# Performance work log

Hardware: AMD Instinct MI355X
Metric: run time of the kernel (lower is better)

## Reference

```python
import jax, jax.numpy as jnp
import numpy as np

EMBED_DIM = 768
NUM_HEADS = 12
HEAD_DIM = EMBED_DIM // NUM_HEADS
SCALE = HEAD_DIM ** -0.5
B, N = 8, 1024


def setup_inputs() -> dict:
    key = jax.random.key(0)
    ks = jax.random.split(key, 5)
    return {
        "x": jax.random.normal(ks[0], (B, N, EMBED_DIM), dtype=jnp.float32),
        "qkv_w": jax.random.normal(ks[1], (3 * EMBED_DIM, EMBED_DIM), dtype=jnp.float32) * 0.02,
        "qkv_b": jax.random.normal(ks[2], (3 * EMBED_DIM,), dtype=jnp.float32) * 0.02,
        "proj_w": jax.random.normal(ks[3], (EMBED_DIM, EMBED_DIM), dtype=jnp.float32) * 0.02,
        "proj_b": jax.random.normal(ks[4], (EMBED_DIM,), dtype=jnp.float32) * 0.02,
    }


def reference(x, qkv_w, qkv_b, proj_w, proj_b):
    b, n, c = x.shape
    h, hd = NUM_HEADS, HEAD_DIM
    # QKV projection: [b,n,3c]
    qkv = jnp.einsum("bnc,dc->bnd", x, qkv_w) + qkv_b
    qkv = qkv.reshape(b, n, 3, h, hd).transpose(2, 0, 3, 1, 4)  # [3,b,h,n,hd]
    q, k, v = qkv[0], qkv[1], qkv[2]
    # scaled dot-product attention (eager path; dropout is identity in eval)
    attn = jnp.einsum("bhqd,bhkd->bhqk", q, k) * SCALE
    attn = jax.nn.softmax(attn, axis=-1)
    out = jnp.einsum("bhqk,bhkd->bhqd", attn, v)  # [b,h,n,hd]
    out = out.transpose(0, 2, 1, 3).reshape(b, n, c)
    # output projection
    return jnp.einsum("bnc,dc->bnd", out, proj_w) + proj_b
```

## Files before the change

### kernel.cpp

```cpp
#include <hip/hip_runtime.h>
#include <hip/hip_bf16.h>

typedef __attribute__((ext_vector_type(4))) float f32x4;
typedef __attribute__((ext_vector_type(8))) short short8;
typedef unsigned short u16;

#define MFMA(a, b, c) __builtin_amdgcn_mfma_f32_16x16x32_bf16((a), (b), (c), 0, 0, 0)

#define WAITVM_BAR(N) do {                                          \
    asm volatile("s_waitcnt vmcnt(" #N ")" ::: "memory");           \
    __builtin_amdgcn_s_barrier();                                   \
    __builtin_amdgcn_sched_barrier(0);                              \
} while (0)
#define BAR2() do {                                                 \
    __builtin_amdgcn_sched_barrier(0);                              \
    __builtin_amdgcn_s_barrier();                                   \
    __builtin_amdgcn_sched_barrier(0);                              \
} while (0)

static constexpr int EMBED = 768;
static constexpr int NH = 12;
static constexpr int HD = 64;
static constexpr int BATCH = 8;
static constexpr int SEQ = 1024;

__device__ __forceinline__ u16 f2bu(float f) {
    __hip_bfloat16 h = __float2bfloat16(f);
    u16 u; __builtin_memcpy(&u, &h, 2); return u;
}
__device__ __forceinline__ float exp2a(float x) {
    float r; asm("v_exp_f32 %0, %1" : "=v"(r) : "v"(x)); return r;
}
__device__ __forceinline__ unsigned cvt_pk_bf16(float lo, float hi) {
    unsigned r; asm("v_cvt_pk_bf16_f32 %0, %1, %2" : "=v"(r) : "v"(lo), "v"(hi)); return r;
}
__device__ __forceinline__ float max3f(float a, float b, float c) {
    return fmaxf(fmaxf(a, b), c);
}
__device__ __forceinline__ void swap32(unsigned& a, unsigned& b) {
    asm volatile("v_permlane32_swap_b32 %0, %1" : "+v"(a), "+v"(b));
}
__device__ __forceinline__ void swap16(unsigned& a, unsigned& b) {
    asm volatile("v_permlane16_swap_b32 %0, %1" : "+v"(a), "+v"(b));
}
__device__ __forceinline__ short8 mk8(unsigned w0, unsigned w1, unsigned w2, unsigned w3) {
    union { unsigned u[4]; short8 s; } c;
    c.u[0] = w0; c.u[1] = w1; c.u[2] = w2; c.u[3] = w3;
    return c.s;
}

__global__ void cvt_all_k(const float* __restrict__ x, const float* __restrict__ w1,
                          const float* __restrict__ w2,
                          u16* __restrict__ xb, u16* __restrict__ wb, u16* __restrict__ pw) {
    const int n1 = BATCH * SEQ * EMBED;
    const int n2 = 3 * EMBED * EMBED;
    const int n3 = EMBED * EMBED;
    int i = (blockIdx.x * blockDim.x + threadIdx.x) * 4;
    const float* src; u16* dst;
    if (i < n1)            { src = x  + i;             dst = xb + i; }
    else if (i < n1 + n2)  { src = w1 + (i - n1);      dst = wb + (i - n1); }
    else if (i < n1+n2+n3) { src = w2 + (i - n1 - n2); dst = pw + (i - n1 - n2); }
    else return;
    float4 v = *reinterpret_cast<const float4*>(src);
    ushort4 o;
    o.x = f2bu(v.x); o.y = f2bu(v.y); o.z = f2bu(v.z); o.w = f2bu(v.w);
    *reinterpret_cast<ushort4*>(dst) = o;
}

template <int EPI>
__global__ __launch_bounds__(256)
void gemm_bt_k(const u16* __restrict__ A, const u16* __restrict__ Bw,
               const float* __restrict__ bias,
               u16* __restrict__ q_out, u16* __restrict__ k_out,
               u16* __restrict__ vt_out, float* __restrict__ f_out)
{
    __shared__ __attribute__((aligned(16))) char smem[65536];
    const int tid  = threadIdx.x;
    const int wave = tid >> 6, lane = tid & 63;
    const int hi   = lane >> 4, l15 = lane & 15;
    const int wr   = wave >> 1, wc = wave & 1;
    const int bm   = blockIdx.x, bn = blockIdx.y;

    f32x4 acc[4][4] = {};

    const size_t arow0 = (size_t)bm * 128;
    const size_t brow0 = (size_t)bn * 128;

    auto stage = [&](int buf, int kt) {
        char* Ab = smem + buf * 32768;
        char* Bb = Ab + 16384;
#pragma unroll
        for (int c = 0; c < 4; ++c) {
            int ck   = c * 4 + wave;
            int p    = ck * 1024 + lane * 16;
            int row  = p >> 7;
            int pcol = (p & 127) ^ ((row & 7) << 4);
            const u16* srcA = A  + (arow0 + row) * EMBED + kt + (pcol >> 1);
            const u16* srcB = Bw + (brow0 + row) * EMBED + kt + (pcol >> 1);
            __builtin_amdgcn_global_load_lds((const __attribute__((address_space(1))) void*)srcA,
                                             (__attribute__((address_space(3))) void*)(Ab + ck * 1024), 16, 0, 0);
            __builtin_amdgcn_global_load_lds((const __attribute__((address_space(1))) void*)srcB,
                                             (__attribute__((address_space(3))) void*)(Bb + ck * 1024), 16, 0, 0);
        }
    };

    auto comp = [&](const char* Ab, const char* Bb) {
#pragma unroll
        for (int kk = 0; kk < 2; ++kk) {
            short8 af[4], bf[4];
#pragma unroll
            for (int mi = 0; mi < 4; ++mi) {
                int R  = wr * 64 + mi * 16 + l15;
                int Cb = kk * 64 + hi * 16;
                af[mi] = *reinterpret_cast<const short8*>(Ab + R * 128 + (Cb ^ ((R & 7) << 4)));
            }
#pragma unroll
            for (int ni = 0; ni < 4; ++ni) {
                int R  = wc * 64 + ni * 16 + l15;
                int Cb = kk * 64 + hi * 16;
                bf[ni] = *reinterpret_cast<const short8*>(Bb + R * 128 + (Cb ^ ((R & 7) << 4)));
            }
#pragma unroll
            for (int mi = 0; mi < 4; ++mi)
#pragma unroll
                for (int ni = 0; ni < 4; ++ni)
                    acc[mi][ni] = MFMA(af[mi], bf[ni], acc[mi][ni]);
        }
    };

    const char* A0 = smem;
    const char* B0 = smem + 16384;
    const char* A1 = smem + 32768;
    const char* B1 = smem + 49152;

    stage(0, 0);
#pragma unroll
    for (int tt = 0; tt < 5; ++tt) {
        stage(1, (2 * tt + 1) * 64);
        WAITVM_BAR(8);
        comp(A0, B0);
        BAR2();
        stage(0, (2 * tt + 2) * 64);
        WAITVM_BAR(8);
        comp(A1, B1);
        BAR2();
    }
    stage(1, 11 * 64);
    WAITVM_BAR(8);
    comp(A0, B0);
    BAR2();
    WAITVM_BAR(0);
    comp(A1, B1);

#pragma unroll
    for (int mi = 0; mi < 4; ++mi) {
        int crow0 = bm * 128 + wr * 64 + mi * 16 + hi * 4;
#pragma unroll
        for (int ni = 0; ni < 4; ++ni) {
            int ccol = bn * 128 + wc * 64 + ni * 16 + l15;
            float bv = bias[ccol];
            if constexpr (EPI == 0) {
                int which = ccol / 768;
                int rem   = ccol - which * 768;
                int hh = rem >> 6, hd = rem & 63;
                int bb = crow0 >> 10, nn0 = crow0 & 1023;
                size_t bh = (size_t)(bb * NH + hh);
                if (which == 2) {
                    uint2 pk;
                    pk.x = cvt_pk_bf16(acc[mi][ni][0] + bv, acc[mi][ni][1] + bv);
                    pk.y = cvt_pk_bf16(acc[mi][ni][2] + bv, acc[mi][ni][3] + bv);
                    *reinterpret_cast<uint2*>(&vt_out[(bh * HD + hd) * SEQ + nn0]) = pk;
                } else if (which == 0) {
#pragma unroll
                    for (int r = 0; r < 4; ++r)
                        q_out[(bh * SEQ + nn0 + r) * HD + hd] =
                            f2bu((acc[mi][ni][r] + bv) * 0.18033688f);
                } else {
#pragma unroll
                    for (int r = 0; r < 4; ++r)
                        k_out[(bh * SEQ + nn0 + r) * HD + hd] = f2bu(acc[mi][ni][r] + bv);
                }
            } else {
#pragma unroll
                for (int r = 0; r < 4; ++r)
                    f_out[(size_t)(crow0 + r) * EMBED + ccol] = acc[mi][ni][r] + bv;
            }
        }
    }
}

__global__ __launch_bounds__(256, 3)
void attn_k(const u16* __restrict__ Q, const u16* __restrict__ K,
            const u16* __restrict__ Vt, u16* __restrict__ AO)
{
    __shared__ __attribute__((aligned(16))) u16 kv[3][8192];

    const int tid = threadIdx.x;
    const int w   = tid >> 6, lane = tid & 63;
    const int hi  = lane >> 4, l15 = lane & 15;
    const int f   = blockIdx.x;
    const int xcd = f & 7, i = f >> 3;
    const int bh  = xcd * 12 + (i % 12);
    const int q0w = (i / 12) * 128 + w * 32;

    const u16* Qh = Q  + (size_t)bh * SEQ * HD;
    const u16* Kh = K  + (size_t)bh * SEQ * HD;
    const u16* Vh = Vt + (size_t)bh * HD * SEQ;

    short8 qf[2][2];
#pragma unroll
    for (int qh = 0; qh < 2; ++qh)
#pragma unroll
        for (int dh = 0; dh < 2; ++dh)
            qf[qh][dh] = *reinterpret_cast<const short8*>(
                Qh + (size_t)(q0w + qh * 16 + l15) * HD + dh * 32 + hi * 8);
    __builtin_amdgcn_sched_barrier(0);

    const u16* sptr[4]; int doff[4]; int sadv[4];
#pragma unroll
    for (int c = 0; c < 4; ++c) {
        int ch = c * 4 + w;
        int mc = ch & 7;
        int p  = mc * 1024 + lane * 16;
        int row = p >> 7;
        int colb = (p & 127) ^ ((row & 7) << 4);
        if (ch < 8) { sptr[c] = Kh + (size_t)row * HD + (colb >> 1); sadv[c] = 64 * HD; doff[c] = mc * 512; }
        else        { sptr[c] = Vh + (size_t)row * SEQ + (colb >> 1); sadv[c] = 64;     doff[c] = 4096 + mc * 512; }
    }
    auto stage = [&](int buf, int t) {
#pragma unroll
        for (int c = 0; c < 4; ++c)
            __builtin_amdgcn_global_load_lds(
                (const __attribute__((address_space(1))) void*)(sptr[c] + (size_t)t * sadv[c]),
                (__attribute__((address_space(3))) void*)(&kv[buf][doff[c]]), 16, 0, 0);
    };

    stage(0, 0);
    stage(1, 1);

    f32x4 accO0[4] = {}, accO1[4] = {};
    float m0 = 0.f, m1 = 0.f, lp0 = 0.f, lp1 = 0.f;

    auto tile = [&](const u16* Kb, const u16* Vb, bool first) {
        f32x4 st0[4] = {}, st1[4] = {};
        __builtin_amdgcn_s_setprio(1);
#pragma unroll
        for (int kb = 0; kb < 4; ++kb) {
            int R  = kb * 16 + l15;
            int sw = (R & 7) << 4;
            short8 kf0 = *reinterpret_cast<const short8*>(Kb + R * 64 + (((hi * 16) ^ sw) >> 1));
            short8 kf1 = *reinterpret_cast<const short8*>(Kb + R * 64 + (((64 + hi * 16) ^ sw) >> 1));
            st0[kb] = MFMA(kf0, qf[0][0], st0[kb]);
            st0[kb] = MFMA(kf1, qf[0][1], st0[kb]);
            st1[kb] = MFMA(kf0, qf[1][0], st1[kb]);
            st1[kb] = MFMA(kf1, qf[1][1], st1[kb]);
        }
        __builtin_amdgcn_s_setprio(0);

        float a0 = max3f(st0[0][0], st0[0][1], st0[0][2]);
        float a1 = max3f(st0[0][3], st0[1][0], st0[1][1]);
        float a2 = max3f(st0[1][2], st0[1][3], st0[2][0]);
        float a3 = max3f(st0[2][1], st0[2][2], st0[2][3]);
        float a4 = max3f(st0[3][0], st0[3][1], st0[3][2]);
        float tm0 = fmaxf(max3f(a0, a1, a2), max3f(a3, a4, st0[3][3]));
        float b0 = max3f(st1[0][0], st1[0][1], st1[0][2]);
        float b1 = max3f(st1[0][3], st1[1][0], st1[1][1]);
        float b2 = max3f(st1[1][2], st1[1][3], st1[2][0]);
        float b3 = max3f(st1[2][1], st1[2][2], st1[2][3]);
        float b4 = max3f(st1[3][0], st1[3][1], st1[3][2]);
        float tm1 = fmaxf(max3f(b0, b1, b2), max3f(b3, b4, st1[3][3]));
        tm0 = fmaxf(tm0, __shfl_xor(tm0, 16, 64));
        tm0 = fmaxf(tm0, __shfl_xor(tm0, 32, 64));
        tm1 = fmaxf(tm1, __shfl_xor(tm1, 16, 64));
        tm1 = fmaxf(tm1, __shfl_xor(tm1, 32, 64));
        if (first) { m0 = tm0; m1 = tm1; }

        unsigned X0[4][2], X1[4][2];
#pragma unroll
        for (int kb = 0; kb < 4; ++kb) {
            float e0 = exp2a(st0[kb][0] - m0);
            float e1 = exp2a(st0[kb][1] - m0);
            float e2 = exp2a(st0[kb][2] - m0);
            float e3 = exp2a(st0[kb][3] - m0);
            lp0 += (e0 + e1) + (e2 + e3);
            X0[kb][0] = cvt_pk_bf16(e0, e1);
            X0[kb][1] = cvt_pk_bf16(e2, e3);
            float g0 = exp2a(st1[kb][0] - m1);
            float g1 = exp2a(st1[kb][1] - m1);
            float g2 = exp2a(st1[kb][2] - m1);
            float g3 = exp2a(st1[kb][3] - m1);
            lp1 += (g0 + g1) + (g2 + g3);
            X1[kb][0] = cvt_pk_bf16(g0, g1);
            X1[kb][1] = cvt_pk_bf16(g2, g3);
        }

        unsigned c0 = X0[0][0], d0 = X0[1][0];
        swap32(c0, d0); swap16(c0, d0);
        unsigned c1 = X0[0][1], d1 = X0[1][1];
        swap32(c1, d1); swap16(c1, d1);
        unsigned c2 = X0[2][0], d2 = X0[3][0];
        swap32(c2, d2); swap16(c2, d2);
        unsigned c3 = X0[2][1], d3 = X0[3][1];
        swap32(c3, d3); swap16(c3, d3);
        short8 pa00 = mk8(c0, c1, d0, d1);
        short8 pa01 = mk8(c2, c3, d2, d3);
        unsigned e0 = X1[0][0], f0 = X1[1][0];
        swap32(e0, f0); swap16(e0, f0);
        unsigned e1 = X1[0][1], f1 = X1[1][1];
        swap32(e1, f1); swap16(e1, f1);
        unsigned e2 = X1[2][0], f2 = X1[3][0];
        swap32(e2, f2); swap16(e2, f2);
        unsigned e3 = X1[2][1], f3 = X1[3][1];
        swap32(e3, f3); swap16(e3, f3);
        short8 pa10 = mk8(e0, e1, f0, f1);
        short8 pa11 = mk8(e2, e3, f2, f3);

        __builtin_amdgcn_s_setprio(1);
#pragma unroll
        for (int db = 0; db < 4; ++db) {
            int R  = db * 16 + l15;
            int sw = (R & 7) << 4;
            short8 vf0 = *reinterpret_cast<const short8*>(Vb + R * 64 + (((hi * 16) ^ sw) >> 1));
            short8 vf1 = *reinterpret_cast<const short8*>(Vb + R * 64 + (((64 + hi * 16) ^ sw) >> 1));
            accO0[db] = MFMA(vf0, pa00, accO0[db]);
            accO0[db] = MFMA(vf1, pa01, accO0[db]);
            accO1[db] = MFMA(vf0, pa10, accO1[db]);
            accO1[db] = MFMA(vf1, pa11, accO1[db]);
        }
        __builtin_amdgcn_s_setprio(0);

        if (!first && !__all((tm0 <= m0 + 8.f) && (tm1 <= m1 + 8.f))) {
            float mn0 = fmaxf(m0, tm0), mn1 = fmaxf(m1, tm1);
            float s0 = exp2a(m0 - mn0), s1 = exp2a(m1 - mn1);
            m0 = mn0; m1 = mn1;
            lp0 *= s0; lp1 *= s1;
#pragma unroll
            for (int db = 0; db < 4; ++db)
#pragma unroll
                for (int r = 0; r < 4; ++r) { accO0[db][r] *= s0; accO1[db][r] *= s1; }
        }
    };

    auto one = [&](int bc, int bs, int tn, bool ds, bool first) {
        asm volatile("s_waitcnt vmcnt(4)" ::: "memory");
        __builtin_amdgcn_s_barrier();
        __builtin_amdgcn_sched_barrier(0);
        if (ds) stage(bs, tn);
        tile(&kv[bc][0], &kv[bc][4096], first);
        __builtin_amdgcn_sched_barrier(0);
    };

    one(0, 2, 2, true, true);
    one(1, 0, 3, true, false);
    one(2, 1, 4, true, false);
    for (int g = 1; g < 5; ++g) {
        one(0, 2, 3 * g + 2, true, false);
        one(1, 0, 3 * g + 3, 3 * g + 3 <= 15, false);
        one(2, 1, 3 * g + 4, 3 * g + 4 <= 15, false);
    }
    asm volatile("s_waitcnt vmcnt(0)" ::: "memory");
    __builtin_amdgcn_s_barrier();
    __builtin_amdgcn_sched_barrier(0);
    tile(&kv[0][0], &kv[0][4096], false);

    lp0 += __shfl_xor(lp0, 16, 64);
    lp0 += __shfl_xor(lp0, 32, 64);
    lp1 += __shfl_xor(lp1, 16, 64);
    lp1 += __shfl_xor(lp1, 32, 64);
    float linv0 = 1.f / lp0, linv1 = 1.f / lp1;
    const int bb = bh / NH, hh = bh - bb * NH;
    size_t rowb0 = ((size_t)bb * SEQ + q0w + l15) * EMBED + hh * HD;
    size_t rowb1 = rowb0 + (size_t)16 * EMBED;
#pragma unroll
    for (int db = 0; db < 4; ++db) {
        uint2 pk0, pk1;
        pk0.x = cvt_pk_bf16(accO0[db][0] * linv0, accO0[db][1] * linv0);
        pk0.y = cvt_pk_bf16(accO0[db][2] * linv0, accO0[db][3] * linv0);
        pk1.x = cvt_pk_bf16(accO1[db][0] * linv1, accO1[db][1] * linv1);
        pk1.y = cvt_pk_bf16(accO1[db][2] * linv1, accO1[db][3] * linv1);
        *reinterpret_cast<uint2*>(&AO[rowb0 + db * 16 + hi * 4]) = pk0;
        *reinterpret_cast<uint2*>(&AO[rowb1 + db * 16 + hi * 4]) = pk1;
    }
}

extern "C" void kernel_launch(void* const* d_in, const int* in_sizes, int n_in,
                              void* d_out, int out_size, void* d_ws, size_t ws_size,
                              hipStream_t stream)
{
    const float* x      = (const float*)d_in[0];
    const float* qkv_w  = (const float*)d_in[1];
    const float* qkv_b  = (const float*)d_in[2];
    const float* proj_w = (const float*)d_in[3];
    const float* proj_b = (const float*)d_in[4];
    float* out = (float*)d_out;

    char* ws = (char*)d_ws;
    u16* xb  = (u16*)(ws);
    u16* wb  = (u16*)(ws + 12582912);
    u16* pw  = (u16*)(ws + 16121856);
    u16* qb  = (u16*)(ws + 17301504);
    u16* kb  = (u16*)(ws + 29884416);
    u16* vt  = (u16*)(ws + 42467328);
    u16* ao  = (u16*)(ws + 55050240);

    cvt_all_k<<<8448, 256, 0, stream>>>(x, qkv_w, proj_w, xb, wb, pw);

    gemm_bt_k<0><<<dim3(64, 18), 256, 0, stream>>>(xb, wb, qkv_b, qb, kb, vt, nullptr);
    attn_k<<<768, 256, 0, stream>>>(qb, kb, vt, ao);
    gemm_bt_k<1><<<dim3(64, 6), 256, 0, stream>>>(ao, pw, proj_b, nullptr, nullptr, nullptr, out);
}
```

Baseline: 103.3 us.

## Switch attention kernel to 32x32x16 bf16 MFMA tiles

The attention kernel now computes QK^T and PV with 32x32x16 MFMA instructions, so each wave handles 32 query rows in one fragment instead of two 16-row fragments. The softmax row-max and row-sum reductions shrink to a single cross-half shuffle, and the P repacking needs only permlane32 swaps. The goal is fewer MFMA issues, fewer K/V LDS fragment reads per FLOP and less softmax bookkeeping. In exchange each lane holds larger accumulator vectors, which raises register pressure, and the fragment and output index mapping must be right for the new layout.

```diff
diff --git a/kernel.cpp b/kernel.cpp
--- a/kernel.cpp
+++ b/kernel.cpp
@@ -2,10 +2,12 @@
 #include <hip/hip_bf16.h>
 
 typedef __attribute__((ext_vector_type(4))) float f32x4;
+typedef __attribute__((ext_vector_type(16))) float f32x16;
 typedef __attribute__((ext_vector_type(8))) short short8;
 typedef unsigned short u16;
 
 #define MFMA(a, b, c) __builtin_amdgcn_mfma_f32_16x16x32_bf16((a), (b), (c), 0, 0, 0)
+#define MFMA32(a, b, c) __builtin_amdgcn_mfma_f32_32x32x16_bf16((a), (b), (c), 0, 0, 0)
 
 #define WAITVM_BAR(N) do {                                          \
     asm volatile("s_waitcnt vmcnt(" #N ")" ::: "memory");           \
@@ -39,9 +41,6 @@
 }
 __device__ __forceinline__ void swap32(unsigned& a, unsigned& b) {
     asm volatile("v_permlane32_swap_b32 %0, %1" : "+v"(a), "+v"(b));
-}
-__device__ __forceinline__ void swap16(unsigned& a, unsigned& b) {
-    asm volatile("v_permlane16_swap_b32 %0, %1" : "+v"(a), "+v"(b));
 }
 __device__ __forceinline__ short8 mk8(unsigned w0, unsigned w1, unsigned w2, unsigned w3) {
     union { unsigned u[4]; short8 s; } c;
@@ -197,7 +196,7 @@
 
     const int tid = threadIdx.x;
     const int w   = tid >> 6, lane = tid & 63;
-    const int hi  = lane >> 4, l15 = lane & 15;
+    const int h   = lane >> 5, l31 = lane & 31;
     const int f   = blockIdx.x;
     const int xcd = f & 7, i = f >> 3;
     const int bh  = xcd * 12 + (i % 12);
@@ -207,13 +206,11 @@
     const u16* Kh = K  + (size_t)bh * SEQ * HD;
     const u16* Vh = Vt + (size_t)bh * HD * SEQ;
 
-    short8 qf[2][2];
-#pragma unroll
-    for (int qh = 0; qh < 2; ++qh)
-#pragma unroll
-        for (int dh = 0; dh < 2; ++dh)
-            qf[qh][dh] = *reinterpret_cast<const short8*>(
-                Qh + (size_t)(q0w + qh * 16 + l15) * HD + dh * 32 + hi * 8);
+    short8 qf[4];
+#pragma unroll
+    for (int ds = 0; ds < 4; ++ds)
+        qf[ds] = *reinterpret_cast<const short8*>(
+            Qh + (size_t)(q0w + l31) * HD + ds * 16 + h * 8);
     __builtin_amdgcn_sched_barrier(0);
 
     const u16* sptr[4]; int doff[4]; int sadv[4];
@@ -238,106 +235,91 @@
     stage(0, 0);
     stage(1, 1);
 
-    f32x4 accO0[4] = {}, accO1[4] = {};
-    float m0 = 0.f, m1 = 0.f, lp0 = 0.f, lp1 = 0.f;
+    f32x16 accO[2] = {};
+    float m = 0.f, lp = 0.f;
 
     auto tile = [&](const u16* Kb, const u16* Vb, bool first) {
-        f32x4 st0[4] = {}, st1[4] = {};
+        f32x16 st[2] = {{0}, {0}};
         __builtin_amdgcn_s_setprio(1);
 #pragma unroll
-        for (int kb = 0; kb < 4; ++kb) {
-            int R  = kb * 16 + l15;
+        for (int mf = 0; mf < 2; ++mf) {
+            int R  = mf * 32 + l31;
             int sw = (R & 7) << 4;
-            short8 kf0 = *reinterpret_cast<const short8*>(Kb + R * 64 + (((hi * 16) ^ sw) >> 1));
-            short8 kf1 = *reinterpret_cast<const short8*>(Kb + R * 64 + (((64 + hi * 16) ^ sw) >> 1));
-            st0[kb] = MFMA(kf0, qf[0][0], st0[kb]);
-            st0[kb] = MFMA(kf1, qf[0][1], st0[kb]);
-            st1[kb] = MFMA(kf0, qf[1][0], st1[kb]);
-            st1[kb] = MFMA(kf1, qf[1][1], st1[kb]);
+#pragma unroll
+            for (int ds = 0; ds < 4; ++ds) {
+                short8 kf = *reinterpret_cast<const short8*>(
+                    Kb + R * 64 + (((ds * 32 + h * 16) ^ sw) >> 1));
+                st[mf] = MFMA32(kf, qf[ds], st[mf]);
+            }
         }
         __builtin_amdgcn_s_setprio(0);
 
-        float a0 = max3f(st0[0][0], st0[0][1], st0[0][2]);
-        float a1 = max3f(st0[0][3], st0[1][0], st0[1][1]);
-        float a2 = max3f(st0[1][2], st0[1][3], st0[2][0]);
-        float a3 = max3f(st0[2][1], st0[2][2], st0[2][3]);
-        float a4 = max3f(st0[3][0], st0[3][1], st0[3][2]);
-        float tm0 = fmaxf(max3f(a0, a1, a2), max3f(a3, a4, st0[3][3]));
-        float b0 = max3f(st1[0][0], st1[0][1], st1[0][2]);
-        float b1 = max3f(st1[0][3], st1[1][0], st1[1][1]);
-        float b2 = max3f(st1[1][2], st1[1][3], st1[2][0]);
-        float b3 = max3f(st1[2][1], st1[2][2], st1[2][3]);
-        float b4 = max3f(st1[3][0], st1[3][1], st1[3][2]);
-        float tm1 = fmaxf(max3f(b0, b1, b2), max3f(b3, b4, st1[3][3]));
-        tm0 = fmaxf(tm0, __shfl_xor(tm0, 16, 64));
-        tm0 = fmaxf(tm0, __shfl_xor(tm0, 32, 64));
-        tm1 = fmaxf(tm1, __shfl_xor(tm1, 16, 64));
-        tm1 = fmaxf(tm1, __shfl_xor(tm1, 32, 64));
-        if (first) { m0 = tm0; m1 = tm1; }
-
-        unsigned X0[4][2], X1[4][2];
-#pragma unroll
-        for (int kb = 0; kb < 4; ++kb) {
-            float e0 = exp2a(st0[kb][0] - m0);
-            float e1 = exp2a(st0[kb][1] - m0);
-            float e2 = exp2a(st0[kb][2] - m0);
-            float e3 = exp2a(st0[kb][3] - m0);
-            lp0 += (e0 + e1) + (e2 + e3);
-            X0[kb][0] = cvt_pk_bf16(e0, e1);
-            X0[kb][1] = cvt_pk_bf16(e2, e3);
-            float g0 = exp2a(st1[kb][0] - m1);
-            float g1 = exp2a(st1[kb][1] - m1);
-            float g2 = exp2a(st1[kb][2] - m1);
-            float g3 = exp2a(st1[kb][3] - m1);
-            lp1 += (g0 + g1) + (g2 + g3);
-            X1[kb][0] = cvt_pk_bf16(g0, g1);
-            X1[kb][1] = cvt_pk_bf16(g2, g3);
-        }
-
-        unsigned c0 = X0[0][0], d0 = X0[1][0];
-        swap32(c0, d0); swap16(c0, d0);
-        unsigned c1 = X0[0][1], d1 = X0[1][1];
-        swap32(c1, d1); swap16(c1, d1);
-        unsigned c2 = X0[2][0], d2 = X0[3][0];
-        swap32(c2, d2); swap16(c2, d2);
-        unsigned c3 = X0[2][1], d3 = X0[3][1];
-        swap32(c3, d3); swap16(c3, d3);
-        short8 pa00 = mk8(c0, c1, d0, d1);
-        short8 pa01 = mk8(c2, c3, d2, d3);
-        unsigned e0 = X1[0][0], f0 = X1[1][0];
-        swap32(e0, f0); swap16(e0, f0);
-        unsigned e1 = X1[0][1], f1 = X1[1][1];
-        swap32(e1, f1); swap16(e1, f1);
-        unsigned e2 = X1[2][0], f2 = X1[3][0];
-        swap32(e2, f2); swap16(e2, f2);
-        unsigned e3 = X1[2][1], f3 = X1[3][1];
-        swap32(e3, f3); swap16(e3, f3);
-        short8 pa10 = mk8(e0, e1, f0, f1);
-        short8 pa11 = mk8(e2, e3, f2, f3);
+        float x0 = max3f(st[0][0],  st[0][1],  st[0][2]);
+        float x1 = max3f(st[0][3],  st[0][4],  st[0][5]);
+        float x2 = max3f(st[0][6],  st[0][7],  st[0][8]);
+        float x3 = max3f(st[0][9],  st[0][10], st[0][11]);
+        float x4 = max3f(st[0][12], st[0][13], st[0][14]);
+        float x5 = max3f(st[0][15], st[1][0],  st[1][1]);
+        float x6 = max3f(st[1][2],  st[1][3],  st[1][4]);
+        float x7 = max3f(st[1][5],  st[1][6],  st[1][7]);
+        float x8 = max3f(st[1][8],  st[1][9],  st[1][10]);
+        float x9 = max3f(st[1][11], st[1][12], st[1][13]);
+        float xa = fmaxf(st[1][14], st[1][15]);
+        float y0 = max3f(x0, x1, x2);
+        float y1 = max3f(x3, x4, x5);
+        float y2 = max3f(x6, x7, x8);
+        float y3 = fmaxf(x9, xa);
+        float tm = fmaxf(max3f(y0, y1, y2), y3);
+        tm = fmaxf(tm, __shfl_xor(tm, 32, 64));
+        if (first) m = tm;
+
+        unsigned pkw[2][8];
+        float s0 = 0.f, s1 = 0.f;
+#pragma unroll
+        for (int mf = 0; mf < 2; ++mf)
+#pragma unroll
+            for (int p = 0; p < 8; ++p) {
+                float e0 = exp2a(st[mf][2 * p]     - m);
+                float e1 = exp2a(st[mf][2 * p + 1] - m);
+                if (mf == 0) s0 += e0 + e1; else s1 += e0 + e1;
+                pkw[mf][p] = cvt_pk_bf16(e0, e1);
+            }
+        lp += s0 + s1;
+
+        short8 pb[4];
+#pragma unroll
+        for (int ks = 0; ks < 4; ++ks) {
+            int mf = ks >> 1, b4 = (ks & 1) * 4;
+            unsigned E0 = pkw[mf][b4 + 0], E1 = pkw[mf][b4 + 1];
+            unsigned D0 = pkw[mf][b4 + 2], D1 = pkw[mf][b4 + 3];
+            swap32(E0, D0);
+            swap32(E1, D1);
+            pb[ks] = mk8(E0, E1, D0, D1);
+        }
 
         __builtin_amdgcn_s_setprio(1);
 #pragma unroll
-        for (int db = 0; db < 4; ++db) {
-            int R  = db * 16 + l15;
+        for (int df = 0; df < 2; ++df) {
+            int R  = df * 32 + l31;
             int sw = (R & 7) << 4;
-            short8 vf0 = *reinterpret_cast<const short8*>(Vb + R * 64 + (((hi * 16) ^ sw) >> 1));
-            short8 vf1 = *reinterpret_cast<const short8*>(Vb + R * 64 + (((64 + hi * 16) ^ sw) >> 1));
-            accO0[db] = MFMA(vf0, pa00, accO0[db]);
-            accO0[db] = MFMA(vf1, pa01, accO0[db]);
-            accO1[db] = MFMA(vf0, pa10, accO1[db]);
-            accO1[db] = MFMA(vf1, pa11, accO1[db]);
+#pragma unroll
+            for (int ks = 0; ks < 4; ++ks) {
+                short8 vf = *reinterpret_cast<const short8*>(
+                    Vb + R * 64 + (((ks * 32 + h * 16) ^ sw) >> 1));
+                accO[df] = MFMA32(vf, pb[ks], accO[df]);
+            }
         }
         __builtin_amdgcn_s_setprio(0);
 
-        if (!first && !__all((tm0 <= m0 + 8.f) && (tm1 <= m1 + 8.f))) {
-            float mn0 = fmaxf(m0, tm0), mn1 = fmaxf(m1, tm1);
-            float s0 = exp2a(m0 - mn0), s1 = exp2a(m1 - mn1);
-            m0 = mn0; m1 = mn1;
-            lp0 *= s0; lp1 *= s1;
-#pragma unroll
-            for (int db = 0; db < 4; ++db)
-#pragma unroll
-                for (int r = 0; r < 4; ++r) { accO0[db][r] *= s0; accO1[db][r] *= s1; }
+        if (!first && !__all(tm <= m + 8.f)) {
+            float mn = fmaxf(m, tm);
+            float s  = exp2a(m - mn);
+            m = mn;
+            lp *= s;
+#pragma unroll
+            for (int df = 0; df < 2; ++df)
+#pragma unroll
+                for (int r = 0; r < 16; ++r) accO[df][r] *= s;
         }
     };
 
@@ -363,24 +345,23 @@
     __builtin_amdgcn_sched_barrier(0);
     tile(&kv[0][0], &kv[0][4096], false);
 
-    lp0 += __shfl_xor(lp0, 16, 64);
-    lp0 += __shfl_xor(lp0, 32, 64);
-    lp1 += __shfl_xor(lp1, 16, 64);
-    lp1 += __shfl_xor(lp1, 32, 64);
-    float linv0 = 1.f / lp0, linv1 = 1.f / lp1;
+    lp += __shfl_xor(lp, 32, 64);
+    float linv = 1.f / lp;
     const int bb = bh / NH, hh = bh - bb * NH;
-    size_t rowb0 = ((size_t)bb * SEQ + q0w + l15) * EMBED + hh * HD;
-    size_t rowb1 = rowb0 + (size_t)16 * EMBED;
-#pragma unroll
-    for (int db = 0; db < 4; ++db) {
-        uint2 pk0, pk1;
-        pk0.x = cvt_pk_bf16(accO0[db][0] * linv0, accO0[db][1] * linv0);
-        pk0.y = cvt_pk_bf16(accO0[db][2] * linv0, accO0[db][3] * linv0);
-        pk1.x = cvt_pk_bf16(accO1[db][0] * linv1, accO1[db][1] * linv1);
-        pk1.y = cvt_pk_bf16(accO1[db][2] * linv1, accO1[db][3] * linv1);
-        *reinterpret_cast<uint2*>(&AO[rowb0 + db * 16 + hi * 4]) = pk0;
-        *reinterpret_cast<uint2*>(&AO[rowb1 + db * 16 + hi * 4]) = pk1;
-    }
+    size_t rowb = ((size_t)bb * SEQ + q0w + l31) * EMBED + hh * HD;
+#pragma unroll
+    for (int df = 0; df < 2; ++df)
+#pragma unroll
+        for (int g = 0; g < 4; ++g) {
+            float o0 = accO[df][4 * g + 0] * linv;
+            float o1 = accO[df][4 * g + 1] * linv;
+            float o2 = accO[df][4 * g + 2] * linv;
+            float o3 = accO[df][4 * g + 3] * linv;
+            uint2 pk;
+            pk.x = cvt_pk_bf16(o0, o1);
+            pk.y = cvt_pk_bf16(o2, o3);
+            *reinterpret_cast<uint2*>(&AO[rowb + df * 32 + 8 * g + 4 * h]) = pk;
+        }
 }
 
 extern "C" void kernel_launch(void* const* d_in, const int* in_sizes, int n_in,
```

New measurement: 103.9 us. No clear change (+0.6%).
